# Kernel optimization log

Measured on AMD Instinct MI355X. Metric: run time of the kernel, lower is better.

Reference implementation:

```python
import jax, jax.numpy as jnp
from jax import lax
import numpy as np

D_MODEL = 1024; N_HEADS = 16; D_K = 64; D_FF = 4096
D_STATE = 16; D_CONV = 4; D_INNER = 2048; EPS = 1e-5
BATCH = 2; SEQ = 2048


def _ln(x, g, b):
    m = x.mean(-1, keepdims=True)
    v = ((x - m) ** 2).mean(-1, keepdims=True)
    return (x - m) * lax.rsqrt(v + EPS) * g + b


def setup_inputs() -> dict:
    key = jax.random.key(0)
    ks = jax.random.split(key, 12)
    rn = lambda k, sh, s=0.02: jax.random.normal(k, sh, jnp.float32) * s
    return {
        'x': jax.random.normal(ks[0], (BATCH, SEQ, D_MODEL), jnp.float32),
        'ln1_g': jnp.ones(D_MODEL), 'ln1_b': jnp.zeros(D_MODEL),
        'Wq': rn(ks[1], (D_MODEL, D_MODEL)), 'bq': jnp.zeros(D_MODEL),
        'Wk': rn(ks[2], (D_MODEL, D_MODEL)), 'bk': jnp.zeros(D_MODEL),
        'Wv': rn(ks[3], (D_MODEL, D_MODEL)), 'bv': jnp.zeros(D_MODEL),
        'Wo': rn(ks[4], (D_MODEL, D_MODEL)), 'bo': jnp.zeros(D_MODEL),
        'ln2_g': jnp.ones(D_MODEL), 'ln2_b': jnp.zeros(D_MODEL),
        'in_w': rn(ks[5], (D_MODEL, 2 * D_INNER)), 'in_b': jnp.zeros(2 * D_INNER),
        'conv_w': rn(ks[6], (D_INNER, 1, D_CONV), 0.2), 'conv_b': jnp.zeros(D_INNER),
        'xp_w': rn(ks[7], (D_INNER, 2 * D_STATE)), 'xp_b': jnp.zeros(2 * D_STATE),
        'dt': rn(ks[8], (D_INNER,), 0.1), 'A': rn(ks[9], (D_STATE, D_STATE), 0.1),
        'Dp': jnp.ones(D_INNER),
        'out_w': rn(ks[10], (D_INNER, D_MODEL)), 'out_b': jnp.zeros(D_MODEL),
        'ln3_g': jnp.ones(D_MODEL), 'ln3_b': jnp.zeros(D_MODEL),
        'fc1_w': rn(ks[11], (D_MODEL, D_FF)), 'fc1_b': jnp.zeros(D_FF),
        'fc2_w': rn(jax.random.fold_in(key, 99), (D_FF, D_MODEL)), 'fc2_b': jnp.zeros(D_MODEL),
    }


def reference(x, ln1_g, ln1_b, Wq, bq, Wk, bk, Wv, bv, Wo, bo, ln2_g, ln2_b,
              in_w, in_b, conv_w, conv_b, xp_w, xp_b, dt, A, Dp, out_w, out_b,
              ln3_g, ln3_b, fc1_w, fc1_b, fc2_w, fc2_b):
    Bsz, S, _ = x.shape
    # --- attention (block sliding-window mask == full causal mask) ---
    h = _ln(x, ln1_g, ln1_b)
    q = (h @ Wq + bq).reshape(Bsz, S, N_HEADS, D_K).transpose(0, 2, 1, 3)
    k = (h @ Wk + bk).reshape(Bsz, S, N_HEADS, D_K).transpose(0, 2, 1, 3)
    v = (h @ Wv + bv).reshape(Bsz, S, N_HEADS, D_K).transpose(0, 2, 1, 3)
    scores = jnp.einsum('bhqd,bhkd->bhqk', q, k) / float(D_K ** 0.5)
    causal = jnp.tril(jnp.ones((S, S), bool))
    scores = jnp.where(causal, scores, -jnp.inf)
    probs = jax.nn.softmax(scores, axis=-1)
    attn = jnp.einsum('bhqk,bhkd->bhqd', probs, v).transpose(0, 2, 1, 3).reshape(Bsz, S, D_MODEL)
    x = x + attn @ Wo + bo
    # --- Mamba-style layer ---
    h = _ln(x, ln2_g, ln2_b)
    xr = h @ in_w + in_b                      # (B,S,2*Di)
    xm, res = xr[..., :D_INNER], xr[..., D_INNER:]
    # causal depthwise conv: torch Conv1d(pad=d_conv-1)[..., :S] == left-pad conv
    xc = lax.conv_general_dilated(xm.transpose(0, 2, 1), conv_w, (1,), [(D_CONV - 1, 0)],
                                  dimension_numbers=('NCH', 'OIH', 'NCH'),
                                  feature_group_count=D_INNER)
    xm = jax.nn.silu((xc + conv_b[None, :, None]).transpose(0, 2, 1))
    xdbl = xm @ xp_w + xp_b                   # (B,S,2*d_state)
    Bm, Cm = xdbl[..., :D_STATE], xdbl[..., D_STATE:]
    # dt = exp(param)[:d_state], indexed by i % d_state per step (as in source)
    dts = jnp.exp(dt)[:D_STATE][jnp.arange(S) % D_STATE]  # (S,)
    # NOTE: the source scan never uses u = x[:,i,:] (and hence D); hs depends
    # only on dt, A, B, C — replicated faithfully here.

    def step(hst, inp):
        d_t, b_t, c_t = inp
        A_t = jnp.exp(d_t * A)                # (d_state,d_state)
        hst = jnp.tanh(hst @ A_t.T) + b_t * hst + c_t
        return hst, hst

    h0 = jnp.zeros((Bsz, D_STATE), x.dtype)
    _, hs = lax.scan(step, h0, (dts, Bm.transpose(1, 0, 2), Cm.transpose(1, 0, 2)))
    hs = hs.transpose(1, 0, 2)                # (B,S,d_state)
    y = jnp.repeat(hs, D_INNER // D_STATE, axis=-1) + res
    x = x + y @ out_w + out_b
    # --- FFN (tanh-approx GELU) ---
    h = _ln(x, ln3_g, ln3_b)
    x = x + jax.nn.gelu(h @ fc1_w + fc1_b, approximate=True) @ fc2_w + fc2_b
    return x
```

## Files before the change

kernel.cpp:

```cpp
#include <hip/hip_runtime.h>
#include <hip/hip_bf16.h>


#define SEQ     2048
#define BATCH   2
#define MROWS   4096
#define DMODEL  1024
#define DINNER  2048
#define DFF     4096
#define QKVLD   3072

typedef __attribute__((ext_vector_type(8))) short bf16x8;
typedef __attribute__((ext_vector_type(4))) float f32x4;
typedef __attribute__((ext_vector_type(2))) __fp16 f16x2;

__device__ __forceinline__ unsigned short f2b(float x){
    __hip_bfloat16 h = __float2bfloat16(x);
    return *reinterpret_cast<unsigned short*>(&h);
}
__device__ __forceinline__ float b2f(unsigned short u){
    __hip_bfloat16 h;
    *reinterpret_cast<unsigned short*>(&h) = u;
    return __bfloat162float(h);
}
__device__ __forceinline__ float gelu_f(float v){
    float u = 0.7978845608f*(v + 0.044715f*v*v*v);
    float e = __expf(2.f*u);
    float th = 1.f - 2.f*__builtin_amdgcn_rcpf(e + 1.f);
    return 0.5f*v*(1.f + th);
}
__device__ __forceinline__ void gload16(const unsigned short* g, unsigned short* l){
    __builtin_amdgcn_global_load_lds(
        (const __attribute__((address_space(1))) void*)g,
        (__attribute__((address_space(3))) void*)l, 16, 0, 0);
}
template<int CTRL>
__device__ __forceinline__ float dppf(float x){
    int r = __builtin_amdgcn_mov_dpp(__builtin_bit_cast(int, x), CTRL, 0xf, 0xf, false);
    return __builtin_bit_cast(float, r);
}
template<int CTRL>
__device__ __forceinline__ int dppi(int x){
    return __builtin_amdgcn_mov_dpp(x, CTRL, 0xf, 0xf, false);
}
template<int CTRL>
__device__ __forceinline__ f16x2 dpp_h2(f16x2 x){
    int r = __builtin_amdgcn_mov_dpp(__builtin_bit_cast(int, x), CTRL, 0xf, 0xf, false);
    return __builtin_bit_cast(f16x2, r);
}

#if __has_builtin(__builtin_amdgcn_exp2f)
#define W_SCALE 2.8853900817779268f
__device__ __forceinline__ float exp_2s(float x){ return __builtin_amdgcn_exp2f(x); }
#else
#define W_SCALE 2.0f
__device__ __forceinline__ float exp_2s(float x){ return __expf(x); }
#endif

__device__ __forceinline__ float hdot2(f16x2 a, f16x2 b, float c){
#if __has_builtin(__builtin_amdgcn_fdot2)
    return __builtin_amdgcn_fdot2(a, b, c, false);
#else
    return c + (float)a[0]*(float)b[0] + (float)a[1]*(float)b[1];
#endif
}

__global__ __launch_bounds__(256) void transpose_cast(
    const float* __restrict__ W, unsigned short* __restrict__ Wt, int K, int N)
{
    __shared__ float t[64*65];
    int n0 = blockIdx.x*64, k0 = blockIdx.y*64;
    int c = threadIdx.x & 63, r0 = threadIdx.x >> 6;
    #pragma unroll
    for (int rr = 0; rr < 64; rr += 4)
        t[(rr+r0)*65 + c] = W[(size_t)(k0+rr+r0)*N + n0 + c];
    __syncthreads();
    #pragma unroll
    for (int rr = 0; rr < 64; rr += 4)
        Wt[(size_t)(n0+rr+r0)*K + k0 + c] = f2b(t[c*65 + rr + r0]);
}

__global__ __launch_bounds__(256) void concat_bias(
    const float* __restrict__ b0, const float* __restrict__ b1,
    const float* __restrict__ b2, float* __restrict__ o)
{
    int t = blockIdx.x*256 + threadIdx.x;
    float v = (t < 1024) ? b0[t] : (t < 2048 ? b1[t-1024] : b2[t-2048]);
    o[t] = v;
}

__global__ __launch_bounds__(256) void layernorm_bf16(
    const float* __restrict__ x, const float* __restrict__ g,
    const float* __restrict__ b, unsigned short* __restrict__ out)
{
    int row = blockIdx.x;
    const float4* xr = (const float4*)(x + (size_t)row*DMODEL);
    int tid = threadIdx.x;
    float4 xv = xr[tid];
    float s  = xv.x + xv.y + xv.z + xv.w;
    float ss = xv.x*xv.x + xv.y*xv.y + xv.z*xv.z + xv.w*xv.w;
    #pragma unroll
    for (int d = 32; d > 0; d >>= 1){ s += __shfl_xor(s,d); ss += __shfl_xor(ss,d); }
    __shared__ float sm[8];
    int wv = tid>>6, ln = tid&63;
    if (ln == 0){ sm[wv] = s; sm[4+wv] = ss; }
    __syncthreads();
    s  = sm[0]+sm[1]+sm[2]+sm[3];
    ss = sm[4]+sm[5]+sm[6]+sm[7];
    float mean = s*(1.f/DMODEL);
    float var  = ss*(1.f/DMODEL) - mean*mean;
    float rstd = rsqrtf(var + 1e-5f);
    float4 gv = ((const float4*)g)[tid];
    float4 bv = ((const float4*)b)[tid];
    ushort4 o;
    o.x = f2b((xv.x-mean)*rstd*gv.x + bv.x);
    o.y = f2b((xv.y-mean)*rstd*gv.y + bv.y);
    o.z = f2b((xv.z-mean)*rstd*gv.z + bv.z);
    o.w = f2b((xv.w-mean)*rstd*gv.w + bv.w);
    ((ushort4*)(out + (size_t)row*DMODEL))[tid] = o;
}

template<int BN, int OUT_BF16, int HAS_RES, int ACT>
__global__ __launch_bounds__(256,3) void gemm_bt(
    const unsigned short* __restrict__ A, const unsigned short* __restrict__ Bt,
    const float* __restrict__ bias, const float* __restrict__ res,
    void* __restrict__ outp, int Ndim, int Kdim)
{
    constexpr int NT = BN/32;
    constexpr int BROWS = BN/32;
    __shared__ unsigned short As[128*64];
    __shared__ unsigned short Bs[BN*64];
    int tid = threadIdx.x;
    int lane = tid & 63, wv = tid >> 6;
    int l15 = lane & 15, quad = lane >> 4;
    int m0 = blockIdx.y*128, n0 = blockIdx.x*BN;
    int mo = (wv>>1)*64, no = (wv&1)*(BN/2);
    int rsub = (lane >> 3);
    int cc8  = (lane & 7)*8;
    f32x4 zz = {0.f,0.f,0.f,0.f};
    f32x4 acc[4][NT];
    #pragma unroll
    for (int i=0;i<4;++i)
      #pragma unroll
      for (int j=0;j<NT;++j) acc[i][j] = zz;

    for (int k0 = 0; k0 < Kdim; k0 += 64){
        const unsigned short* Ab = A  + (size_t)(m0 + wv*32 + rsub)*Kdim + k0 + cc8;
        const unsigned short* Bb = Bt + (size_t)(n0 + wv*(BN/4) + rsub)*Kdim + k0 + cc8;
        #pragma unroll
        for (int i=0;i<4;++i)
            gload16(Ab + (size_t)(i*8)*Kdim, &As[(wv*32 + i*8)*64]);
        #pragma unroll
        for (int i=0;i<BROWS;++i)
            gload16(Bb + (size_t)(i*8)*Kdim, &Bs[(wv*(BN/4) + i*8)*64]);
        __syncthreads();
        #pragma unroll
        for (int kc=0;kc<2;++kc){
            bf16x8 af[4], bfr[NT];
            #pragma unroll
            for (int t=0;t<4;++t)
                af[t]  = *(const bf16x8*)(&As[(mo + t*16 + l15)*64 + kc*32 + quad*8]);
            #pragma unroll
            for (int t=0;t<NT;++t)
                bfr[t] = *(const bf16x8*)(&Bs[(no + t*16 + l15)*64 + kc*32 + quad*8]);
            #pragma unroll
            for (int mt=0;mt<4;++mt)
              #pragma unroll
              for (int nt=0;nt<NT;++nt)
                acc[mt][nt] = __builtin_amdgcn_mfma_f32_16x16x32_bf16(af[mt], bfr[nt], acc[mt][nt], 0,0,0);
        }
        __syncthreads();
    }
    #pragma unroll
    for (int mt=0;mt<4;++mt){
      #pragma unroll
      for (int nt=0;nt<NT;++nt){
        int gn = n0 + no + nt*16 + l15;
        float bval = bias[gn];
        #pragma unroll
        for (int r=0;r<4;++r){
            int gm = m0 + mo + mt*16 + quad*4 + r;
            size_t off = (size_t)gm*Ndim + gn;
            float v = acc[mt][nt][r] + bval;
            if constexpr (HAS_RES) v += res[off];
            if constexpr (ACT == 1) v = gelu_f(v);
            if constexpr (OUT_BF16) ((unsigned short*)outp)[off] = f2b(v);
            else                    ((float*)outp)[off] = v;
        }
      }
    }
}

__global__ __launch_bounds__(256) void transpose_v(
    const unsigned short* __restrict__ qkv, unsigned short* __restrict__ vT)
{
    __shared__ unsigned int t[64*33];
    int bh = blockIdx.y;
    int t0 = blockIdx.x*64;
    int tid = threadIdx.x;
    const size_t base = (size_t)(bh>>4)*SEQ*QKVLD + (size_t)(bh&15)*64 + 2*DMODEL;
    #pragma unroll
    for (int i=0;i<2;++i){
        int idx = tid + i*256;
        int r = idx>>3, cc = idx&7;
        uint4 vv = *(const uint4*)(qkv + base + (size_t)(t0+r)*QKVLD + cc*8);
        t[r*33 + cc*4 + 0] = vv.x;
        t[r*33 + cc*4 + 1] = vv.y;
        t[r*33 + cc*4 + 2] = vv.z;
        t[r*33 + cc*4 + 3] = vv.w;
    }
    __syncthreads();
    unsigned short* outb = vT + (size_t)bh*64*SEQ + t0;
    #pragma unroll
    for (int i=0;i<2;++i){
        int idx = tid + i*256;
        int d = idx>>3, cc = idx&7;
        int sh = (d&1)*16, dp = d>>1;
        unsigned int o4[4];
        #pragma unroll
        for (int j2=0;j2<4;++j2){
            unsigned int ua = t[(cc*8 + 2*j2    )*33 + dp];
            unsigned int ub = t[(cc*8 + 2*j2 + 1)*33 + dp];
            unsigned int ha = (ua >> sh) & 0xffff;
            unsigned int hb = (ub >> sh) & 0xffff;
            o4[j2] = ha | (hb << 16);
        }
        *(uint4*)(outb + (size_t)d*SEQ + cc*8) = *(uint4*)o4;
    }
}

__device__ __forceinline__ void stage_kv(
    const unsigned short* __restrict__ k, const unsigned short* __restrict__ vTb,
    int t0, unsigned short* Ks, unsigned short* Vt, int wv, int lane)
{
    #pragma unroll
    for (int p=0;p<4;++p){
        int c0 = p*256 + wv*64;
        int c  = c0 + lane;
        int kr = c>>3, kc = (c&7)*8;
        int vr = c>>4, vc = (c&15)*8;
        gload16(k   + (size_t)(t0+kr)*QKVLD + (kc ^ ((kr&7)<<3)), Ks + c0*8);
        gload16(vTb + (size_t)vr*SEQ + t0 +   (vc ^ ((vr&7)<<3)), Vt + c0*8);
    }
}

__global__ __launch_bounds__(256,2) void attn_flash(
    const unsigned short* __restrict__ qkv, const unsigned short* __restrict__ vT,
    unsigned short* __restrict__ attn)
{
    __shared__ unsigned short Ks[128*64];
    __shared__ unsigned short Vt[64*128];
    __shared__ unsigned short Ps[64*136];
    int bh = blockIdx.y;
    int qt = (int)gridDim.x - 1 - (int)blockIdx.x;
    int q0 = qt*128;
    int tid = threadIdx.x, wv = tid>>6, lane = tid&63;
    int l15 = lane&15, quad = lane>>4;
    int xsw = (l15&7)<<3;
    const size_t basei = (size_t)(bh>>4)*SEQ*QKVLD + (size_t)(bh&15)*64;
    const unsigned short* q = qkv + basei;
    const unsigned short* k = qkv + basei + DMODEL;
    const unsigned short* vTb = vT + (size_t)bh*64*SEQ;
    const size_t baseo = (size_t)(bh>>4)*SEQ*DMODEL + (size_t)(bh&15)*64;

    int nkt = qt + 1;

    stage_kv(k, vTb, 0, Ks, Vt, wv, lane);

    bf16x8 aq[2][2];
    #pragma unroll
    for (int s=0;s<2;++s){
        int qr = q0 + wv*32 + s*16 + l15;
        aq[s][0] = *(const bf16x8*)(q + (size_t)qr*QKVLD + quad*8);
        aq[s][1] = *(const bf16x8*)(q + (size_t)qr*QKVLD + 32 + quad*8);
    }

    float m_i[2][4], l_i[2][4];
    f32x4 zz = {0.f,0.f,0.f,0.f};
    f32x4 o[2][4];
    #pragma unroll
    for (int s=0;s<2;++s)
      #pragma unroll
      for (int r=0;r<4;++r){ m_i[s][r] = -__builtin_inff(); l_i[s][r] = 0.f; }
    #pragma unroll
    for (int s=0;s<2;++s)
      #pragma unroll
      for (int d=0;d<4;++d) o[s][d] = zz;

    const float SCL = 0.1803368801111137f;

    __syncthreads();

    for (int kt = 0; kt < nkt; ++kt){
        int t0 = kt*128;
        bool diagt = (kt == qt);

        #pragma unroll
        for (int sub=0; sub<2; ++sub){
            f32x4 sc[8];
            #pragma unroll
            for (int st=0;st<8;++st){
                bf16x8 b0 = *(const bf16x8*)(&Ks[(st*16+l15)*64 + ((     quad*8) ^ xsw)]);
                bf16x8 b1 = *(const bf16x8*)(&Ks[(st*16+l15)*64 + ((32 + quad*8) ^ xsw)]);
                sc[st] = __builtin_amdgcn_mfma_f32_16x16x32_bf16(aq[sub][0], b0, zz, 0,0,0);
                sc[st] = __builtin_amdgcn_mfma_f32_16x16x32_bf16(aq[sub][1], b1, sc[st], 0,0,0);
            }
            int qrb = q0 + wv*32 + sub*16 + quad*4;
            float mrow[4];
            #pragma unroll
            for (int r=0;r<4;++r) mrow[r] = -__builtin_inff();
            #pragma unroll
            for (int st=0;st<8;++st)
              #pragma unroll
              for (int r=0;r<4;++r){
                float svv = sc[st][r]*SCL;
                if (diagt && (t0 + st*16 + l15 > qrb + r))
                    svv = -__builtin_inff();
                sc[st][r] = svv;
                mrow[r] = fmaxf(mrow[r], svv);
              }
            #pragma unroll
            for (int d=1; d<16; d<<=1)
              #pragma unroll
              for (int r=0;r<4;++r) mrow[r] = fmaxf(mrow[r], __shfl_xor(mrow[r], d));
            float alpha[4], rsum[4];
            #pragma unroll
            for (int r=0;r<4;++r){
                float mn = fmaxf(m_i[sub][r], mrow[r]);
                alpha[r] = exp_2s(m_i[sub][r] - mn);
                m_i[sub][r] = mn;
            }
            #pragma unroll
            for (int st=0;st<8;++st)
              #pragma unroll
              for (int r=0;r<4;++r) sc[st][r] = exp_2s(sc[st][r] - m_i[sub][r]);
            #pragma unroll
            for (int r=0;r<4;++r){
                rsum[r] = ((sc[0][r]+sc[1][r])+(sc[2][r]+sc[3][r]))
                        + ((sc[4][r]+sc[5][r])+(sc[6][r]+sc[7][r]));
            }
            #pragma unroll
            for (int d=1; d<16; d<<=1)
              #pragma unroll
              for (int r=0;r<4;++r) rsum[r] += __shfl_xor(rsum[r], d);
            #pragma unroll
            for (int r=0;r<4;++r) l_i[sub][r] = l_i[sub][r]*alpha[r] + rsum[r];
            #pragma unroll
            for (int st=0;st<8;++st)
              #pragma unroll
              for (int r=0;r<4;++r)
                Ps[(wv*16 + quad*4 + r)*136 + st*16 + l15] = f2b(sc[st][r]);
            #pragma unroll
            for (int d=0;d<4;++d)
              #pragma unroll
              for (int r=0;r<4;++r) o[sub][d][r] = o[sub][d][r]*alpha[r];

            bf16x8 ap[4];
            #pragma unroll
            for (int kch=0;kch<4;++kch)
                ap[kch] = *(const bf16x8*)(&Ps[(wv*16 + l15)*136 + kch*32 + quad*8]);
            #pragma unroll
            for (int dtile=0;dtile<4;++dtile){
                #pragma unroll
                for (int kch=0;kch<4;++kch){
                    bf16x8 bv_ = *(const bf16x8*)(&Vt[(dtile*16+l15)*128 + ((kch*32 + quad*8) ^ xsw)]);
                    o[sub][dtile] = __builtin_amdgcn_mfma_f32_16x16x32_bf16(ap[kch], bv_, o[sub][dtile], 0,0,0);
                }
            }
        }

        if (kt + 1 < nkt){
            __syncthreads();
            stage_kv(k, vTb, t0 + 128, Ks, Vt, wv, lane);
            __syncthreads();
        }
    }
    #pragma unroll
    for (int sub=0; sub<2; ++sub)
      #pragma unroll
      for (int r=0;r<4;++r){
        float inv = 1.f/l_i[sub][r];
        int gm = q0 + wv*32 + sub*16 + quad*4 + r;
        #pragma unroll
        for (int dtile=0;dtile<4;++dtile)
            attn[baseo + (size_t)gm*DMODEL + dtile*16 + l15] = f2b(o[sub][dtile][r]*inv);
      }
}

__global__ __launch_bounds__(256) void conv_silu(
    const unsigned short* __restrict__ xr, const float* __restrict__ cw,
    const float* __restrict__ cb, unsigned short* __restrict__ xm2)
{
    int idx = blockIdx.x*256 + threadIdx.x;
    int r  = idx >> 10;
    int c2 = (idx & 1023)*2;
    int s  = r & (SEQ-1);
    float4 w0 = *(const float4*)(cw + c2*4);
    float4 w1 = *(const float4*)(cw + (c2+1)*4);
    float w0a[4] = {w0.x,w0.y,w0.z,w0.w};
    float w1a[4] = {w1.x,w1.y,w1.z,w1.w};
    float a0 = cb[c2], a1 = cb[c2+1];
    const unsigned short* xrow = xr + (size_t)r*DFF + c2;
    #pragma unroll
    for (int j=0;j<4;++j){
        int sp = s - 3 + j;
        if (sp >= 0){
            int off = (j-3)*DFF;
            unsigned int u = *(const unsigned int*)(xrow + off);
            a0 += w0a[j]*b2f(u & 0xffff);
            a1 += w1a[j]*b2f(u >> 16);
        }
    }
    float s0 = a0 * __builtin_amdgcn_rcpf(1.f + __expf(-a0));
    float s1 = a1 * __builtin_amdgcn_rcpf(1.f + __expf(-a1));
    unsigned int op = (unsigned int)f2b(s0) | ((unsigned int)f2b(s1) << 16);
    *(unsigned int*)(xm2 + (size_t)r*DINNER + c2) = op;
}

__global__ __launch_bounds__(256) void xp_gemm(
    const unsigned short* __restrict__ xm2, const float* __restrict__ w,
    const float* __restrict__ bias, float* __restrict__ xdbl)
{
    int tid = threadIdx.x;
    int lr = tid >> 5, n = tid & 31;
    int row = blockIdx.x*8 + lr;
    const unsigned short* ar = xm2 + (size_t)row*DINNER;
    float acc = bias[n];
    #pragma unroll 4
    for (int k2 = 0; k2 < DINNER; k2 += 2){
        unsigned int u = *(const unsigned int*)(ar + k2);
        acc += b2f(u & 0xffff)*w[k2*32 + n] + b2f(u >> 16)*w[(k2+1)*32 + n];
    }
    if (n >= 16) acc += 1.f;
    int nc = (n < 16) ? 2*n : 2*(n-16)+1;
    xdbl[(size_t)row*32 + nc] = acc;
}

__device__ __forceinline__ float scan_step_dot(float h, const f16x2 (&Wp)[8],
                                               float bv, float cv)
{
    float rr = dppf<0x121>(h);
    f16x2 p0 = __builtin_amdgcn_cvt_pkrtz(h, rr);
    f16x2 p1 = dpp_h2<0x122>(p0);
    f16x2 p2 = dpp_h2<0x124>(p0);
    f16x2 p3 = dpp_h2<0x126>(p0);
    f16x2 p4 = dpp_h2<0x128>(p0);
    f16x2 p5 = dpp_h2<0x12a>(p0);
    f16x2 p6 = dpp_h2<0x12c>(p0);
    f16x2 p7 = dpp_h2<0x12e>(p0);
    float a0 = hdot2(Wp[0], p0, 0.f);
    a0 = hdot2(Wp[1], p1, a0);
    a0 = hdot2(Wp[2], p2, a0);
    a0 = hdot2(Wp[3], p3, a0);
    float a1 = hdot2(Wp[4], p4, 0.f);
    a1 = hdot2(Wp[5], p5, a1);
    a1 = hdot2(Wp[6], p6, a1);
    a1 = hdot2(Wp[7], p7, a1);
    float u  = fmaf(bv, h, cv);
    float e2 = exp_2s(a0 + a1);
    float r  = __builtin_amdgcn_rcpf(e2 + 1.f);
    return fmaf(-2.f, r, u);
}

__device__ __forceinline__ void load_bank(float2 (&bk)[16], const float* src){
    #pragma unroll
    for (int j=0;j<16;++j) bk[j] = *(const float2*)(src + (size_t)j*32);
}

__device__ __forceinline__ void compute16(const float2 (&bk)[16],
                                          const f16x2 (&Wf)[16][8],
                                          float& hn, float* hp, int lane)
{
    float h0s=0.f, h1s=0.f, h2s=0.f;
    #pragma unroll
    for (int j=0;j<16;++j){
        hn = scan_step_dot(hn, Wf[j], bk[j].x, bk[j].y);
        if ((j&3)==0)      h0s = hn;
        else if ((j&3)==1) h1s = hn;
        else if ((j&3)==2) h2s = hn;
        else if (lane < 16){
            float4 o4 = {h0s, h1s, h2s, hn};
            *(float4*)(hp + j - 3) = o4;
        }
    }
}

__global__ __launch_bounds__(128,1) void scan_k(
    const float* __restrict__ xdbl, const float* __restrict__ dt,
    const float* __restrict__ A, float* __restrict__ hsT)
{
    int tid = threadIdx.x;
    int lane = tid & 63;
    int b = tid >> 6;
    int i = lane & 15;

    int c1 = dppi<0x121>(i);
    int sj[8], tj[8];
    sj[0] = i;               tj[0] = c1;
    sj[1] = dppi<0x122>(i);  tj[1] = dppi<0x122>(c1);
    sj[2] = dppi<0x124>(i);  tj[2] = dppi<0x124>(c1);
    sj[3] = dppi<0x126>(i);  tj[3] = dppi<0x126>(c1);
    sj[4] = dppi<0x128>(i);  tj[4] = dppi<0x128>(c1);
    sj[5] = dppi<0x12a>(i);  tj[5] = dppi<0x12a>(c1);
    sj[6] = dppi<0x12c>(i);  tj[6] = dppi<0x12c>(c1);
    sj[7] = dppi<0x12e>(i);  tj[7] = dppi<0x12e>(c1);

    f16x2 Wf[16][8];
    #pragma unroll
    for (int p=0;p<16;++p){
        float dtp = __expf(dt[p]);
        #pragma unroll
        for (int jj=0;jj<8;++jj){
            float w0 = W_SCALE*__expf(dtp * A[i*16 + sj[jj]]);
            float w1 = W_SCALE*__expf(dtp * A[i*16 + tj[jj]]);
            Wf[p][jj] = __builtin_amdgcn_cvt_pkrtz(w0, w1);
        }
    }

    const float* src = xdbl + (size_t)(b*SEQ)*32 + 2*i;
    float* hp = hsT + (size_t)(b*16 + i)*SEQ;
    float2 bA[16], bB[16];
    load_bank(bA, src);
    float hn = 0.f;
    for (int bp = 0; bp < 64; ++bp){
        int t0 = bp*32;
        load_bank(bB, src + (size_t)(t0+16)*32);
        compute16(bA, Wf, hn, hp + t0, lane);
        int t2 = (bp < 63) ? (t0 + 32) : 0;
        load_bank(bA, src + (size_t)t2*32);
        compute16(bB, Wf, hn, hp + t0 + 16, lane);
    }
}

__global__ __launch_bounds__(256) void y_assemble(
    const float* __restrict__ hsT, const unsigned short* __restrict__ xr,
    unsigned short* __restrict__ y)
{
    int idx = blockIdx.x*256 + threadIdx.x;
    int r = idx >> 10;
    int c2 = (idx & 1023)*2;
    int bb = r >> 11, s = r & (SEQ-1);
    unsigned int u = *(const unsigned int*)(xr + (size_t)r*DFF + DINNER + c2);
    float h0 = hsT[(size_t)(bb*16 + (c2 >> 7))*SEQ + s];
    float y0 = h0 + b2f(u & 0xffff);
    float y1 = h0 + b2f(u >> 16);
    *(unsigned int*)(y + (size_t)r*DINNER + c2) =
        (unsigned int)f2b(y0) | ((unsigned int)f2b(y1) << 16);
}

extern "C" void kernel_launch(void* const* d_in, const int* in_sizes, int n_in,
                              void* d_out, int out_size, void* d_ws, size_t ws_size,
                              hipStream_t stream)
{
    (void)in_sizes; (void)n_in; (void)out_size; (void)ws_size;
    const float* x     = (const float*)d_in[0];
    const float* ln1_g = (const float*)d_in[1];
    const float* ln1_b = (const float*)d_in[2];
    const float* Wq    = (const float*)d_in[3];
    const float* bq    = (const float*)d_in[4];
    const float* Wk    = (const float*)d_in[5];
    const float* bk    = (const float*)d_in[6];
    const float* Wv    = (const float*)d_in[7];
    const float* bv    = (const float*)d_in[8];
    const float* Wo    = (const float*)d_in[9];
    const float* bo    = (const float*)d_in[10];
    const float* ln2_g = (const float*)d_in[11];
    const float* ln2_b = (const float*)d_in[12];
    const float* in_w  = (const float*)d_in[13];
    const float* in_b  = (const float*)d_in[14];
    const float* conv_w= (const float*)d_in[15];
    const float* conv_b= (const float*)d_in[16];
    const float* xp_w  = (const float*)d_in[17];
    const float* xp_b  = (const float*)d_in[18];
    const float* dt    = (const float*)d_in[19];
    const float* A     = (const float*)d_in[20];
    const float* out_w = (const float*)d_in[22];
    const float* out_b = (const float*)d_in[23];
    const float* ln3_g = (const float*)d_in[24];
    const float* ln3_b = (const float*)d_in[25];
    const float* fc1_w = (const float*)d_in[26];
    const float* fc1_b = (const float*)d_in[27];
    const float* fc2_w = (const float*)d_in[28];
    const float* fc2_b = (const float*)d_in[29];

    char* ws = (char*)d_ws;
    const size_t MB = 1ull << 20;
    unsigned short* qkvT = (unsigned short*)(ws + 0*MB);
    unsigned short* WoT  = (unsigned short*)(ws + 6*MB);
    unsigned short* inT  = (unsigned short*)(ws + 8*MB);
    unsigned short* outT = (unsigned short*)(ws + 16*MB);
    unsigned short* f1T  = (unsigned short*)(ws + 20*MB);
    unsigned short* f2T  = (unsigned short*)(ws + 28*MB);
    unsigned short* hbf  = (unsigned short*)(ws + 36*MB);
    float*          x2   = (float*)(ws + 44*MB);
    float*          x3   = (float*)(ws + 60*MB);
    unsigned short* qkv  = (unsigned short*)(ws + 76*MB);
    unsigned short* attnb= (unsigned short*)(ws + 100*MB);
    unsigned short* xr   = (unsigned short*)(ws + 76*MB);
    unsigned short* ffn  = (unsigned short*)(ws + 76*MB);
    unsigned short* xm2  = (unsigned short*)(ws + 108*MB);
    unsigned short* yb   = (unsigned short*)(ws + 108*MB);
    float*          xdbl = (float*)(ws + 124*MB);
    float*          hsb  = (float*)(ws + 124*MB + 512*1024);
    float*          bqkv = (float*)(ws + 125*MB);

    dim3 blk(256);
    transpose_cast<<<dim3(16,16), blk, 0, stream>>>(Wq, qkvT,              1024, 1024);
    transpose_cast<<<dim3(16,16), blk, 0, stream>>>(Wk, qkvT + 1024*1024,  1024, 1024);
    transpose_cast<<<dim3(16,16), blk, 0, stream>>>(Wv, qkvT + 2*1024*1024,1024, 1024);
    transpose_cast<<<dim3(16,16), blk, 0, stream>>>(Wo, WoT, 1024, 1024);
    transpose_cast<<<dim3(64,16), blk, 0, stream>>>(in_w, inT, 1024, 4096);
    transpose_cast<<<dim3(16,32), blk, 0, stream>>>(out_w, outT, 2048, 1024);
    transpose_cast<<<dim3(64,16), blk, 0, stream>>>(fc1_w, f1T, 1024, 4096);
    transpose_cast<<<dim3(16,64), blk, 0, stream>>>(fc2_w, f2T, 4096, 1024);
    concat_bias<<<12, blk, 0, stream>>>(bq, bk, bv, bqkv);

    layernorm_bf16<<<MROWS, blk, 0, stream>>>(x, ln1_g, ln1_b, hbf);
    gemm_bt<128,1,0,0><<<dim3(24,32), blk, 0, stream>>>(hbf, qkvT, bqkv, nullptr, qkv, QKVLD, 1024);
    transpose_v<<<dim3(32,32), blk, 0, stream>>>(qkv, hbf);
    attn_flash<<<dim3(16,32), blk, 0, stream>>>(qkv, hbf, attnb);
    gemm_bt<64,0,1,0><<<dim3(16,32), blk, 0, stream>>>(attnb, WoT, bo, x, x2, 1024, 1024);
    layernorm_bf16<<<MROWS, blk, 0, stream>>>(x2, ln2_g, ln2_b, hbf);
    gemm_bt<128,1,0,0><<<dim3(32,32), blk, 0, stream>>>(hbf, inT, in_b, nullptr, xr, 4096, 1024);
    conv_silu<<<16384, blk, 0, stream>>>(xr, conv_w, conv_b, xm2);
    xp_gemm<<<512, blk, 0, stream>>>(xm2, xp_w, xp_b, xdbl);
    scan_k<<<1, dim3(128), 0, stream>>>(xdbl, dt, A, hsb);
    y_assemble<<<16384, blk, 0, stream>>>(hsb, xr, yb);
    gemm_bt<64,0,1,0><<<dim3(16,32), blk, 0, stream>>>(yb, outT, out_b, x2, x3, 1024, 2048);
    layernorm_bf16<<<MROWS, blk, 0, stream>>>(x3, ln3_g, ln3_b, hbf);
    gemm_bt<128,1,0,1><<<dim3(32,32), blk, 0, stream>>>(hbf, f1T, fc1_b, nullptr, ffn, 4096, 1024);
    gemm_bt<64,0,1,0><<<dim3(16,32), blk, 0, stream>>>(ffn, f2T, fc2_b, x3, (float*)d_out, 1024, 4096);
}
```

Measured before the change: 859.7 us.

## Double-buffer K/V tiles in flash attention and swizzle P staging buffer

The attention kernel now keeps two shared-memory K/V buffers and issues the async global loads for the next key tile before computing on the current one. Partial vmcnt waits and raw barriers replace the full syncthreads pair, so load latency can overlap with the MFMA work. The P scratch buffer drops its padded stride of 136 in favour of an XOR swizzle to avoid bank conflicts. LDS per block grows from about 49KB to about 80KB, which may reduce occupancy below the two blocks per CU requested in the launch bounds. The hand-counted vmcnt(8) wait also has to match the exact number of outstanding loads.

```diff
diff --git a/kernel.cpp b/kernel.cpp
--- a/kernel.cpp
+++ b/kernel.cpp
@@ -248,9 +248,9 @@
     const unsigned short* __restrict__ qkv, const unsigned short* __restrict__ vT,
     unsigned short* __restrict__ attn)
 {
-    __shared__ unsigned short Ks[128*64];
-    __shared__ unsigned short Vt[64*128];
-    __shared__ unsigned short Ps[64*136];
+    __shared__ unsigned short Ks[2][128*64];
+    __shared__ unsigned short Vt[2][64*128];
+    __shared__ unsigned short Ps[64*128];
     int bh = blockIdx.y;
     int qt = (int)gridDim.x - 1 - (int)blockIdx.x;
     int q0 = qt*128;
@@ -265,7 +265,7 @@
 
     int nkt = qt + 1;
 
-    stage_kv(k, vTb, 0, Ks, Vt, wv, lane);
+    stage_kv(k, vTb, 0, Ks[0], Vt[0], wv, lane);
 
     bf16x8 aq[2][2];
     #pragma unroll
@@ -289,19 +289,32 @@
 
     const float SCL = 0.1803368801111137f;
 
-    __syncthreads();
+    asm volatile("s_waitcnt vmcnt(0)" ::: "memory");
+    __builtin_amdgcn_s_barrier();
 
     for (int kt = 0; kt < nkt; ++kt){
         int t0 = kt*128;
         bool diagt = (kt == qt);
+        int cur = kt & 1;
+        const unsigned short* Kc = Ks[cur];
+        const unsigned short* Vc = Vt[cur];
+
+        if (kt + 1 < nkt){
+            stage_kv(k, vTb, t0 + 128, Ks[cur^1], Vt[cur^1], wv, lane);
+            asm volatile("s_waitcnt vmcnt(8)" ::: "memory");
+        } else {
+            asm volatile("s_waitcnt vmcnt(0)" ::: "memory");
+        }
+        __builtin_amdgcn_sched_barrier(0);
+        __builtin_amdgcn_s_barrier();
 
         #pragma unroll
         for (int sub=0; sub<2; ++sub){
             f32x4 sc[8];
             #pragma unroll
             for (int st=0;st<8;++st){
-                bf16x8 b0 = *(const bf16x8*)(&Ks[(st*16+l15)*64 + ((     quad*8) ^ xsw)]);
-                bf16x8 b1 = *(const bf16x8*)(&Ks[(st*16+l15)*64 + ((32 + quad*8) ^ xsw)]);
+                bf16x8 b0 = *(const bf16x8*)(&Kc[(st*16+l15)*64 + ((     quad*8) ^ xsw)]);
+                bf16x8 b1 = *(const bf16x8*)(&Kc[(st*16+l15)*64 + ((32 + quad*8) ^ xsw)]);
                 sc[st] = __builtin_amdgcn_mfma_f32_16x16x32_bf16(aq[sub][0], b0, zz, 0,0,0);
                 sc[st] = __builtin_amdgcn_mfma_f32_16x16x32_bf16(aq[sub][1], b1, sc[st], 0,0,0);
             }
@@ -348,8 +361,10 @@
             #pragma unroll
             for (int st=0;st<8;++st)
               #pragma unroll
-              for (int r=0;r<4;++r)
-                Ps[(wv*16 + quad*4 + r)*136 + st*16 + l15] = f2b(sc[st][r]);
+              for (int r=0;r<4;++r){
+                int prow = wv*16 + quad*4 + r;
+                Ps[prow*128 + ((st*16 + l15) ^ (((quad*4+r)&7)<<3))] = f2b(sc[st][r]);
+              }
             #pragma unroll
             for (int d=0;d<4;++d)
               #pragma unroll
@@ -358,22 +373,18 @@
             bf16x8 ap[4];
             #pragma unroll
             for (int kch=0;kch<4;++kch)
-                ap[kch] = *(const bf16x8*)(&Ps[(wv*16 + l15)*136 + kch*32 + quad*8]);
+                ap[kch] = *(const bf16x8*)(&Ps[(wv*16 + l15)*128 + ((kch*32 + quad*8) ^ xsw)]);
             #pragma unroll
             for (int dtile=0;dtile<4;++dtile){
                 #pragma unroll
                 for (int kch=0;kch<4;++kch){
-                    bf16x8 bv_ = *(const bf16x8*)(&Vt[(dtile*16+l15)*128 + ((kch*32 + quad*8) ^ xsw)]);
+                    bf16x8 bv_ = *(const bf16x8*)(&Vc[(dtile*16+l15)*128 + ((kch*32 + quad*8) ^ xsw)]);
                     o[sub][dtile] = __builtin_amdgcn_mfma_f32_16x16x32_bf16(ap[kch], bv_, o[sub][dtile], 0,0,0);
                 }
             }
         }
 
-        if (kt + 1 < nkt){
-            __syncthreads();
-            stage_kv(k, vTb, t0 + 128, Ks, Vt, wv, lane);
-            __syncthreads();
-        }
+        __builtin_amdgcn_s_barrier();
     }
     #pragma unroll
     for (int sub=0; sub<2; ++sub)
```

Result: no change. 858.9 us (-0.1%).
